# Performance work log

Measured on AMD Instinct MI355X. Metric: run time of the kernel, lower is better.

The kernel has to match this reference:

```python
import jax, jax.numpy as jnp
import numpy as np

# Circuit structure constants (match init_kwargs)
N_NODES = 32768        # number of sum nodes in this layer
N_CHILD = 65536        # number of child nodes
NNZ = 1048576          # number of sparse weight entries (avg fan-in 32)
BATCH = 128


def setup_inputs() -> dict:
    key = jax.random.key(0)
    k1, k2, k3, k4 = jax.random.split(key, 4)
    # child log-likelihoods per sample (output of child layers)
    child_ll = jax.random.normal(k1, (BATCH, N_CHILD), dtype=jnp.float32)
    # sparse log-weights of the BCOO weight matrix [N_NODES, N_CHILD]
    log_w = jax.random.normal(k2, (NNZ,), dtype=jnp.float32)
    rows = jnp.sort(jax.random.randint(k3, (NNZ,), 0, N_NODES)).astype(jnp.int64)
    cols = jax.random.randint(k4, (NNZ,), 0, N_CHILD).astype(jnp.int64)
    return {"child_ll": child_ll, "log_w": log_w, "rows": rows, "cols": cols}


def reference(child_ll, log_w, rows, cols):
    """Faithful jax translation of SumLayer.log_likelihood_of_nodes.

    Original: per sample, exponentiate BCOO log-weights and child
    log-likelihoods, sparse matvec (weights @ exp(child_ll)), then
    log(result) - log_normalization_constants, where the normalization
    constants are log(row-sums of exp(log_weights)).
    """
    w = jnp.exp(log_w)  # [NNZ]
    # log normalization constants: log of row-sums of exp(log_weights)
    log_z = jnp.log(jax.ops.segment_sum(w, rows, num_segments=N_NODES))  # [N_NODES]

    def per_sample(ll):  # ll: [N_CHILD]
        p = jnp.exp(ll)
        contrib = w * p[cols]                                   # gather + weight [NNZ]
        return jax.ops.segment_sum(contrib, rows, num_segments=N_NODES)  # [N_NODES]

    s = jax.vmap(per_sample)(child_ll)  # [BATCH, N_NODES]
    return jnp.log(s) - log_z
```

## Files before the change

### kernel.cpp

```cpp
#include <hip/hip_runtime.h>
#include <hip/hip_fp16.h>
#include <math.h>

#define BATCH     128
#define N_NODES   32768
#define N_CHILD   65536
#define NNZ_TOTAL 1048576

__global__ __launch_bounds__(256) void exp_transpose_kernel(
    const float* __restrict__ child_ll, __half* __restrict__ ex) {
    __shared__ float tile[64][BATCH + 1];
    const int c0 = blockIdx.x * 64;
    const int t  = threadIdx.x;

    {
        const int cl = t & 63;
        const int b0 = t >> 6;
#pragma unroll
        for (int j = 0; j < BATCH / 4; ++j) {
            const int b = b0 + j * 4;
            tile[cl][b] = expf(child_ll[(size_t)b * N_CHILD + c0 + cl]);
        }
    }
    __syncthreads();

    {
        const int cl = t >> 4;
        const int b0 = (t & 15) * 8;
#pragma unroll
        for (int p = 0; p < 4; ++p) {
            const int c = p * 16 + cl;
            union { __half2 h[4]; uint4 u; } pk;
#pragma unroll
            for (int k = 0; k < 4; ++k)
                pk.h[k] = __half2{__float2half(tile[c][b0 + 2 * k]),
                                  __float2half(tile[c][b0 + 2 * k + 1])};
            *(uint4*)&ex[(size_t)(c0 + c) * BATCH + b0] = pk.u;
        }
    }
}

__global__ __launch_bounds__(256) void exp_w_kernel(
    const float* __restrict__ log_w, float* __restrict__ w) {
    const int i = (blockIdx.x * 256 + threadIdx.x) * 4;
    float4 v = *(const float4*)&log_w[i];
    v.x = expf(v.x); v.y = expf(v.y); v.z = expf(v.z); v.w = expf(v.w);
    *(float4*)&w[i] = v;
}

__global__ __launch_bounds__(256) void row_starts_kernel(
    const int* __restrict__ rows, int* __restrict__ row_start) {
    const int r = blockIdx.x * blockDim.x + threadIdx.x;
    if (r > N_NODES) return;
    if (r == N_NODES) { row_start[r] = NNZ_TOTAL; return; }
    int lo = 0, hi = NNZ_TOTAL;
    while (lo < hi) {
        const int mid = (lo + hi) >> 1;
        if (rows[mid] < r) lo = mid + 1; else hi = mid;
    }
    row_start[r] = lo;
}

__global__ __launch_bounds__(256, 4) void sum_rows_kernel(
    const __half* __restrict__ ex, const float* __restrict__ w,
    const int* __restrict__ cols, const int* __restrict__ row_start,
    float* __restrict__ out) {
    const int wave = threadIdx.x >> 6;
    const int lane = threadIdx.x & 63;
    const int bid  = blockIdx.x;
    const int rb   = (bid & 7) * (N_NODES / 4 / 8) + (bid >> 3);
    const int r    = rb * 4 + wave;

    const int start = row_start[r];
    const int end   = row_start[r + 1];
    const char* exb = (const char*)ex;
    const unsigned bo = (unsigned)lane * 4u;

    float accx = 0.f, accy = 0.f, wlane = 0.f;

    for (int base = start; base < end; base += 64) {
        const int  idx   = base + lane;
        const bool valid = idx < end;
        const int  cidx  = valid ? idx : start;
        const int  c     = __builtin_nontemporal_load(&cols[cidx]);
        const float wv   = valid ? __builtin_nontemporal_load(&w[idx]) : 0.f;
        wlane += wv;
        const int seg = end - base;

        __half2 ga[16], gb[16];

#pragma unroll
        for (int jj = 0; jj < 16; ++jj) {
            const unsigned cj = (unsigned)__builtin_amdgcn_readlane(c, jj);
            ga[jj] = *(const __half2*)(exb + ((size_t)cj << 8) + bo);
        }

#pragma unroll
        for (int t16 = 0; t16 < 4; ++t16) {
            if (t16 < 3 && (t16 + 1) * 16 < seg) {
#pragma unroll
                for (int jj = 0; jj < 16; ++jj) {
                    const int j = (t16 + 1) * 16 + jj;
                    const unsigned cj = (unsigned)__builtin_amdgcn_readlane(c, j);
                    gb[jj] = *(const __half2*)(exb + ((size_t)cj << 8) + bo);
                }
            }
            if (t16 * 16 < seg) {
#pragma unroll
                for (int jj = 0; jj < 16; ++jj) {
                    const int j = t16 * 16 + jj;
                    const float wj = __uint_as_float(
                        __builtin_amdgcn_readlane(__float_as_uint(wv), j));
                    const __half2 g = ga[jj];
                    accx = fmaf(wj, __half2float(__low2half(g)), accx);
                    accy = fmaf(wj, __half2float(__high2half(g)), accy);
                }
            }
#pragma unroll
            for (int jj = 0; jj < 16; ++jj) ga[jj] = gb[jj];
        }
    }

    float wsum = wlane;
#pragma unroll
    for (int m = 1; m < 64; m <<= 1) wsum += __shfl_xor(wsum, m, 64);
    const float logz = logf(wsum);

    const int b = lane * 2;
    out[(size_t)b * N_NODES + r]       = logf(accx) - logz;
    out[(size_t)(b + 1) * N_NODES + r] = logf(accy) - logz;
}

extern "C" void kernel_launch(void* const* d_in, const int* in_sizes, int n_in,
                              void* d_out, int out_size, void* d_ws, size_t ws_size,
                              hipStream_t stream) {
    const float* child_ll = (const float*)d_in[0];
    const float* log_w    = (const float*)d_in[1];
    const int*   rows     = (const int*)d_in[2];
    const int*   cols     = (const int*)d_in[3];
    float*       out      = (float*)d_out;

    __half* ex        = (__half*)d_ws;
    float*  w         = (float*)((char*)d_ws + (size_t)N_CHILD * BATCH * 2);
    int*    row_start = (int*)((char*)w + (size_t)NNZ_TOTAL * 4);

    exp_transpose_kernel<<<N_CHILD / 64, 256, 0, stream>>>(child_ll, ex);
    exp_w_kernel<<<NNZ_TOTAL / 1024, 256, 0, stream>>>(log_w, w);
    row_starts_kernel<<<(N_NODES + 256) / 256 + 1, 256, 0, stream>>>(rows, row_start);
    sum_rows_kernel<<<N_NODES / 4, 256, 0, stream>>>(ex, w, cols, row_start, out);
}
```

Measured before the change: 67.44 us.

## Gather 16-byte batch chunks per lane, splitting a wave across four nonzeros

Restructures the sparse gather so each lane loads a 16-byte uint4 (8 half batch values) instead of a 4-byte half2. The wave is split into four 16-lane groups, each handling a different nonzero, with column and weight broadcast via ds_bpermute instead of scalar readlane. Eight partial accumulators per lane are reduced across the groups with xor shuffles at the end, and only 16 lanes write the outputs. This cuts the number of gather instructions per nonzero, but adds LDS permute traffic, more registers, and leaves the 48 reducing lanes idle at the output step.

```diff
diff --git a/kernel.cpp b/kernel.cpp
--- a/kernel.cpp
+++ b/kernel.cpp
@@ -74,61 +74,88 @@
     const int start = row_start[r];
     const int end   = row_start[r + 1];
     const char* exb = (const char*)ex;
-    const unsigned bo = (unsigned)lane * 4u;
+    const unsigned bo = ((unsigned)lane & 15u) * 16u;
+    const int pbase = (lane >> 4) * 4;
 
-    float accx = 0.f, accy = 0.f, wlane = 0.f;
+    float acc[8] = {0.f, 0.f, 0.f, 0.f, 0.f, 0.f, 0.f, 0.f};
+    float wlane = 0.f;
 
     for (int base = start; base < end; base += 64) {
         const int  idx   = base + lane;
         const bool valid = idx < end;
-        const int  cidx  = valid ? idx : start;
-        const int  c     = __builtin_nontemporal_load(&cols[cidx]);
-        const float wv   = valid ? __builtin_nontemporal_load(&w[idx]) : 0.f;
+        const int   c  = __builtin_nontemporal_load(&cols[valid ? idx : start]);
+        const float wv = valid ? __builtin_nontemporal_load(&w[idx]) : 0.f;
         wlane += wv;
         const int seg = end - base;
 
-        __half2 ga[16], gb[16];
+#pragma unroll
+        for (int h = 0; h < 2; ++h) {
+            const int hb = h * 32;
+            if (hb >= seg) break;
+
+            int  ct[8];
+            float wt[8];
+            uint4 g[8];
 
 #pragma unroll
-        for (int jj = 0; jj < 16; ++jj) {
-            const unsigned cj = (unsigned)__builtin_amdgcn_readlane(c, jj);
-            ga[jj] = *(const __half2*)(exb + ((size_t)cj << 8) + bo);
-        }
-
+            for (int q = 0; q < 4; ++q) {
+                if (hb + q * 8 < seg) {
 #pragma unroll
-        for (int t16 = 0; t16 < 4; ++t16) {
-            if (t16 < 3 && (t16 + 1) * 16 < seg) {
-#pragma unroll
-                for (int jj = 0; jj < 16; ++jj) {
-                    const int j = (t16 + 1) * 16 + jj;
-                    const unsigned cj = (unsigned)__builtin_amdgcn_readlane(c, j);
-                    gb[jj] = *(const __half2*)(exb + ((size_t)cj << 8) + bo);
-                }
-            }
-            if (t16 * 16 < seg) {
-#pragma unroll
-                for (int jj = 0; jj < 16; ++jj) {
-                    const int j = t16 * 16 + jj;
-                    const float wj = __uint_as_float(
-                        __builtin_amdgcn_readlane(__float_as_uint(wv), j));
-                    const __half2 g = ga[jj];
-                    accx = fmaf(wj, __half2float(__low2half(g)), accx);
-                    accy = fmaf(wj, __half2float(__high2half(g)), accy);
+                    for (int u = 0; u < 2; ++u) {
+                        const int t = q * 2 + u;
+                        const int pa = pbase + (hb + 4 * t) * 4;
+                        ct[t] = __builtin_amdgcn_ds_bpermute(pa, c);
+                        wt[t] = __uint_as_float(__builtin_amdgcn_ds_bpermute(
+                            pa, __float_as_uint(wv)));
+                    }
                 }
             }
 #pragma unroll
-            for (int jj = 0; jj < 16; ++jj) ga[jj] = gb[jj];
+            for (int q = 0; q < 4; ++q) {
+                if (hb + q * 8 < seg) {
+#pragma unroll
+                    for (int u = 0; u < 2; ++u) {
+                        const int t = q * 2 + u;
+                        g[t] = *(const uint4*)(exb +
+                                ((size_t)(unsigned)ct[t] << 8) + bo);
+                    }
+                }
+            }
+#pragma unroll
+            for (int q = 0; q < 4; ++q) {
+                if (hb + q * 8 < seg) {
+#pragma unroll
+                    for (int u = 0; u < 2; ++u) {
+                        const int t = q * 2 + u;
+                        const __half2* hp = (const __half2*)&g[t];
+#pragma unroll
+                        for (int k = 0; k < 4; ++k) {
+                            const float2 f = __half22float2(hp[k]);
+                            acc[2 * k]     = fmaf(wt[t], f.x, acc[2 * k]);
+                            acc[2 * k + 1] = fmaf(wt[t], f.y, acc[2 * k + 1]);
+                        }
+                    }
+                }
+            }
         }
     }
 
+#pragma unroll
+    for (int k = 0; k < 8; ++k) {
+        acc[k] += __shfl_xor(acc[k], 16, 64);
+        acc[k] += __shfl_xor(acc[k], 32, 64);
+    }
     float wsum = wlane;
 #pragma unroll
     for (int m = 1; m < 64; m <<= 1) wsum += __shfl_xor(wsum, m, 64);
     const float logz = logf(wsum);
 
-    const int b = lane * 2;
-    out[(size_t)b * N_NODES + r]       = logf(accx) - logz;
-    out[(size_t)(b + 1) * N_NODES + r] = logf(accy) - logz;
+    if (lane < 16) {
+        const int b0 = lane * 8;
+#pragma unroll
+        for (int k = 0; k < 8; ++k)
+            out[(size_t)(b0 + k) * N_NODES + r] = logf(acc[k]) - logz;
+    }
 }
 
 extern "C" void kernel_launch(void* const* d_in, const int* in_sizes, int n_in,
```

After: 69.04 us. +2.4%, slower.
